# Kernel optimization log

Hardware: AMD Instinct MI355X
Metric: run time of the kernel (lower is better)

Reference implementation:

```python
import jax, jax.numpy as jnp
import numpy as np

TEMPERATURE = 8.0  # sqrt(d_k) with d_k = 64


def setup_inputs() -> dict:
    key = jax.random.key(0)
    k1, k2, k3, k4 = jax.random.split(key, 4)
    B, S, D = 16, 2048, 64  # B = batch * n_heads
    q = jax.random.normal(k1, (B, S, D), dtype=jnp.float32)
    k = jax.random.normal(k2, (B, S, D), dtype=jnp.float32)
    v = jax.random.normal(k3, (B, S, D), dtype=jnp.float32)
    # boolean mask: True = masked out. Low prob so no row is fully masked.
    mask = jax.random.uniform(k4, (B, S, S)) < 0.1
    return {"q": q, "k": k, "v": v, "mask": mask}


def reference(q, k, v, mask):
    # attn = (q @ k^T) / temperature, masked_fill(mask, -inf), softmax over last dim
    attn = jnp.einsum("bqd,bkd->bqk", q, k) / TEMPERATURE
    attn = jnp.where(mask, -jnp.inf, attn)
    attn = jax.nn.softmax(attn, axis=2)
    output = jnp.einsum("bqk,bkd->bqd", attn, v)
    return output, attn
```

## Files before the change

### kernel.cpp

```cpp
#include <hip/hip_runtime.h>

typedef _Float16 half8 __attribute__((ext_vector_type(8)));
typedef _Float16 half4 __attribute__((ext_vector_type(4)));
typedef float    floatx4 __attribute__((ext_vector_type(4)));

#define NB  16
#define SEQ 2048
#define DIM 64

#define MFMA(a,b,c) __builtin_amdgcn_mfma_f32_16x16x32_f16((a),(b),(c),0,0,0)

__global__ __launch_bounds__(256) void cvt_qk_kernel(const float* __restrict__ q,
                                                     const float* __restrict__ k,
                                                     _Float16* __restrict__ qh,
                                                     _Float16* __restrict__ kh) {
    size_t i = ((size_t)blockIdx.x * 256 + threadIdx.x) * 4;
    float4 a = *(const float4*)(q + i);
    float4 b = *(const float4*)(k + i);
    half4 ha = { (_Float16)a.x, (_Float16)a.y, (_Float16)a.z, (_Float16)a.w };
    half4 hb = { (_Float16)b.x, (_Float16)b.y, (_Float16)b.z, (_Float16)b.w };
    *(half4*)(qh + i) = ha;
    *(half4*)(kh + i) = hb;
}

__global__ __launch_bounds__(256) void cvt_vt_kernel(const float* __restrict__ v,
                                                     _Float16* __restrict__ vt) {
    __shared__ float tile[64][65];
    const int b  = blockIdx.x >> 5;
    const int s0 = (blockIdx.x & 31) << 6;
    const int t  = threadIdx.x;
    {
        const int row = t >> 2;
        const int c0  = (t & 3) << 4;
        const float* src = v + ((size_t)(b * SEQ + s0 + row)) * DIM + c0;
        #pragma unroll
        for (int i = 0; i < 4; ++i) {
            float4 x = *(const float4*)(src + i * 4);
            tile[row][c0 + i*4 + 0] = x.x;
            tile[row][c0 + i*4 + 1] = x.y;
            tile[row][c0 + i*4 + 2] = x.z;
            tile[row][c0 + i*4 + 3] = x.w;
        }
    }
    __syncthreads();
    {
        const int d  = t >> 2;
        const int sb = (t & 3) << 4;
        _Float16* dst = vt + ((size_t)(b * DIM + d)) * SEQ + s0 + sb;
        #pragma unroll
        for (int i = 0; i < 4; ++i) {
            half4 h = { (_Float16)tile[sb + i*4 + 0][d],
                        (_Float16)tile[sb + i*4 + 1][d],
                        (_Float16)tile[sb + i*4 + 2][d],
                        (_Float16)tile[sb + i*4 + 3][d] };
            *(half4*)(dst + i*4) = h;
        }
    }
}

__global__ __launch_bounds__(256) void mask_bits_kernel(const int* __restrict__ mask,
                                                        unsigned int* __restrict__ bits) {
    const int wave = threadIdx.x >> 6;
    const int lane = threadIdx.x & 63;
    const size_t row = (size_t)blockIdx.x * 4 + wave;
    const int* mp = mask + row * SEQ + lane;
    unsigned int keep = 0;
    #pragma unroll
    for (int it = 0; it < 32; ++it) {
        int m = __builtin_nontemporal_load(mp + it * 64);
        unsigned long long bal = __ballot(m != 0);
        unsigned int half = (lane & 1) ? (unsigned int)(bal >> 32) : (unsigned int)bal;
        if ((lane >> 1) == it) keep = half;
    }
    bits[row * 64 + lane] = keep;
}

__global__ __launch_bounds__(256, 8) void attn_kernel(
    const _Float16* __restrict__ qh, const _Float16* __restrict__ kh,
    const _Float16* __restrict__ vt, const unsigned int* __restrict__ bits,
    float* __restrict__ out, float* __restrict__ attn)
{
    __shared__ float wsum[4][16];
    __shared__ __align__(16) unsigned char lds_u[4 * 16 * 68 * 4];
    _Float16* tsc    = (_Float16*)lds_u;
    float*    outred = (float*)lds_u;

    const int b    = blockIdx.x >> 7;
    const int r0   = (blockIdx.x & 127) << 4;
    const int lane = threadIdx.x & 63;
    const int wave = threadIdx.x >> 6;
    const int rl   = lane & 15;
    const int g    = lane >> 4;

    const size_t qoff = ((size_t)(b * SEQ + r0 + rl)) * DIM + g * 8;
    const half8 qa0 = *(const half8*)(qh + qoff);
    const half8 qa1 = *(const half8*)(qh + qoff + 32);

    const _Float16* kbase = kh + (size_t)b * SEQ * DIM + (size_t)rl * DIM + g * 8;
    const unsigned int* bbase = bits + ((size_t)(b * SEQ + r0 + rl)) * 64 + wave;

    float rs = 0.f;
    unsigned int pb = bbase[0];

    for (int cc = 0; cc < 16; ++cc) {
        const int jj = (cc * 4 + wave) * 32;
        const unsigned int bm = pb;
        if (cc < 15) pb = bbase[(cc + 1) * 4];
        const _Float16* kp = kbase + (size_t)jj * DIM;
        half8 ka0 = *(const half8*)(kp);
        half8 ka1 = *(const half8*)(kp + 32);
        half8 kb0 = *(const half8*)(kp + 16 * DIM);
        half8 kb1 = *(const half8*)(kp + 16 * DIM + 32);
        floatx4 c0 = {0.f,0.f,0.f,0.f}, c1 = {0.f,0.f,0.f,0.f};
        c0 = MFMA(ka0, qa0, c0);
        c0 = MFMA(ka1, qa1, c0);
        c1 = MFMA(kb0, qa0, c1);
        c1 = MFMA(kb1, qa1, c1);
        const unsigned int blo = bm >> (g * 4);
        const unsigned int bhi = bm >> (g * 4 + 16);
        float e0 = (blo & 1u) ? 0.f : __expf(c0[0] * 0.125f);
        float e1 = (blo & 2u) ? 0.f : __expf(c0[1] * 0.125f);
        float e2 = (blo & 4u) ? 0.f : __expf(c0[2] * 0.125f);
        float e3 = (blo & 8u) ? 0.f : __expf(c0[3] * 0.125f);
        float e4 = (bhi & 1u) ? 0.f : __expf(c1[0] * 0.125f);
        float e5 = (bhi & 2u) ? 0.f : __expf(c1[1] * 0.125f);
        float e6 = (bhi & 4u) ? 0.f : __expf(c1[2] * 0.125f);
        float e7 = (bhi & 8u) ? 0.f : __expf(c1[3] * 0.125f);
        rs += (e0 + e1) + (e2 + e3) + (e4 + e5) + (e6 + e7);
    }

    rs += __shfl_xor(rs, 16);
    rs += __shfl_xor(rs, 32);
    if (g == 0) wsum[wave][rl] = rs;
    __syncthreads();
    const float inv = 1.0f / (wsum[0][rl] + wsum[1][rl] + wsum[2][rl] + wsum[3][rl]);

    floatx4 o0 = {0.f,0.f,0.f,0.f}, o1 = {0.f,0.f,0.f,0.f};
    floatx4 o2 = {0.f,0.f,0.f,0.f}, o3 = {0.f,0.f,0.f,0.f};
    const _Float16* vbase = vt + ((size_t)b * DIM + rl) * SEQ + g * 8;
    float* abase = attn + ((size_t)(b * SEQ + r0 + rl)) * SEQ + g * 4;
    _Float16* trow = tsc + (wave * 16 + rl) * 40;

    for (int cc = 0; cc < 16; ++cc) {
        const int jj = (cc * 4 + wave) * 32;
        const unsigned int bm = bbase[cc * 4];
        const _Float16* kp = kbase + (size_t)jj * DIM;
        half8 ka0 = *(const half8*)(kp);
        half8 ka1 = *(const half8*)(kp + 32);
        half8 kb0 = *(const half8*)(kp + 16 * DIM);
        half8 kb1 = *(const half8*)(kp + 16 * DIM + 32);
        floatx4 c0 = {0.f,0.f,0.f,0.f}, c1 = {0.f,0.f,0.f,0.f};
        c0 = MFMA(ka0, qa0, c0);
        c0 = MFMA(ka1, qa1, c0);
        c1 = MFMA(kb0, qa0, c1);
        c1 = MFMA(kb1, qa1, c1);

        const unsigned int blo = bm >> (g * 4);
        const unsigned int bhi = bm >> (g * 4 + 16);
        float e0 = (blo & 1u) ? 0.f : __expf(c0[0] * 0.125f);
        float e1 = (blo & 2u) ? 0.f : __expf(c0[1] * 0.125f);
        float e2 = (blo & 4u) ? 0.f : __expf(c0[2] * 0.125f);
        float e3 = (blo & 8u) ? 0.f : __expf(c0[3] * 0.125f);
        float e4 = (bhi & 1u) ? 0.f : __expf(c1[0] * 0.125f);
        float e5 = (bhi & 2u) ? 0.f : __expf(c1[1] * 0.125f);
        float e6 = (bhi & 4u) ? 0.f : __expf(c1[2] * 0.125f);
        float e7 = (bhi & 8u) ? 0.f : __expf(c1[3] * 0.125f);

        floatx4 a0 = { e0 * inv, e1 * inv, e2 * inv, e3 * inv };
        floatx4 a1 = { e4 * inv, e5 * inv, e6 * inv, e7 * inv };
        *(floatx4*)(abase + jj)      = a0;
        *(floatx4*)(abase + jj + 16) = a1;

        half4 h0 = { (_Float16)e0, (_Float16)e1, (_Float16)e2, (_Float16)e3 };
        half4 h1 = { (_Float16)e4, (_Float16)e5, (_Float16)e6, (_Float16)e7 };
        *(half4*)(trow + g * 4)      = h0;
        *(half4*)(trow + 16 + g * 4) = h1;
        half8 eb = *(const half8*)(trow + g * 8);

        const _Float16* vp = vbase + jj;
        half8 v0 = *(const half8*)(vp);
        half8 v1 = *(const half8*)(vp + 16 * SEQ);
        half8 v2 = *(const half8*)(vp + 32 * SEQ);
        half8 v3 = *(const half8*)(vp + 48 * SEQ);
        o0 = MFMA(v0, eb, o0);
        o1 = MFMA(v1, eb, o1);
        o2 = MFMA(v2, eb, o2);
        o3 = MFMA(v3, eb, o3);
    }

    __syncthreads();
    {
        float* orow = outred + (wave * 16 + rl) * 68 + g * 4;
        *(floatx4*)(orow +  0) = o0;
        *(floatx4*)(orow + 16) = o1;
        *(floatx4*)(orow + 32) = o2;
        *(floatx4*)(orow + 48) = o3;
    }
    __syncthreads();
    {
        const int r  = threadIdx.x >> 4;
        const int c4 = (threadIdx.x & 15) << 2;
        floatx4 s0 = *(const floatx4*)(outred + ( 0 + r) * 68 + c4);
        floatx4 s1 = *(const floatx4*)(outred + (16 + r) * 68 + c4);
        floatx4 s2 = *(const floatx4*)(outred + (32 + r) * 68 + c4);
        floatx4 s3 = *(const floatx4*)(outred + (48 + r) * 68 + c4);
        floatx4 s = (s0 + s1) + (s2 + s3);
        const float inv2 = 1.0f / (wsum[0][r] + wsum[1][r] + wsum[2][r] + wsum[3][r]);
        floatx4 ov = { s[0] * inv2, s[1] * inv2, s[2] * inv2, s[3] * inv2 };
        *(floatx4*)(out + ((size_t)(b * SEQ + r0 + r)) * DIM + c4) = ov;
    }
}

extern "C" void kernel_launch(void* const* d_in, const int* in_sizes, int n_in,
                              void* d_out, int out_size, void* d_ws, size_t ws_size,
                              hipStream_t stream) {
    const float* q = (const float*)d_in[0];
    const float* k = (const float*)d_in[1];
    const float* v = (const float*)d_in[2];
    const int* mask = (const int*)d_in[3];

    float* out  = (float*)d_out;
    float* attn = out + (size_t)NB * SEQ * DIM;

    _Float16* qh = (_Float16*)d_ws;
    _Float16* kh = qh + (size_t)NB * SEQ * DIM;
    _Float16* vt = kh + (size_t)NB * SEQ * DIM;
    unsigned int* bits = (unsigned int*)(vt + (size_t)NB * SEQ * DIM);

    cvt_qk_kernel<<<(NB * SEQ * DIM) / 1024, 256, 0, stream>>>(q, k, qh, kh);
    cvt_vt_kernel<<<NB * (SEQ / 64), 256, 0, stream>>>(v, vt);
    mask_bits_kernel<<<(NB * SEQ) / 4, 256, 0, stream>>>(mask, bits);
    attn_kernel<<<NB * (SEQ / 16), 256, 0, stream>>>(qh, kh, vt, bits, out, attn);
}
```

Baseline: 623.8 us.

## Move PV accumulation into first pass using 16x16x16 MFMA, drop LDS transpose

The P·V product is now accumulated in the first (row-sum) pass, with unnormalized fp16 exponentials fed directly from the QK accumulator layout into 16x16x16 MFMAs. This removes the per-iteration LDS round-trip that shuffled scores into operand layout, and leaves the second pass only writing normalized attention probabilities. It also remaps block indices so neighbouring blocks take different batches, and lowers the occupancy hint from 8 to 6. In exchange it uses more registers and twice as many smaller MFMA instructions, and the first pass now also loads V.

```diff
diff --git a/kernel.cpp b/kernel.cpp
--- a/kernel.cpp
+++ b/kernel.cpp
@@ -8,7 +8,8 @@
 #define SEQ 2048
 #define DIM 64
 
-#define MFMA(a,b,c) __builtin_amdgcn_mfma_f32_16x16x32_f16((a),(b),(c),0,0,0)
+#define MFMA32(a,b,c) __builtin_amdgcn_mfma_f32_16x16x32_f16((a),(b),(c),0,0,0)
+#define MFMA16(a,b,c) __builtin_amdgcn_mfma_f32_16x16x16f16((a),(b),(c),0,0,0)
 
 __global__ __launch_bounds__(256) void cvt_qk_kernel(const float* __restrict__ q,
                                                      const float* __restrict__ k,
@@ -75,18 +76,17 @@
     bits[row * 64 + lane] = keep;
 }
 
-__global__ __launch_bounds__(256, 8) void attn_kernel(
+__global__ __launch_bounds__(256, 6) void attn_kernel(
     const _Float16* __restrict__ qh, const _Float16* __restrict__ kh,
     const _Float16* __restrict__ vt, const unsigned int* __restrict__ bits,
     float* __restrict__ out, float* __restrict__ attn)
 {
     __shared__ float wsum[4][16];
-    __shared__ __align__(16) unsigned char lds_u[4 * 16 * 68 * 4];
-    _Float16* tsc    = (_Float16*)lds_u;
-    float*    outred = (float*)lds_u;
-
-    const int b    = blockIdx.x >> 7;
-    const int r0   = (blockIdx.x & 127) << 4;
+    __shared__ __align__(16) float outred[4][16][68];
+
+    const int blk  = ((blockIdx.x & 7) << 8) + (blockIdx.x >> 3);
+    const int b    = blk >> 7;
+    const int r0   = (blk & 127) << 4;
     const int lane = threadIdx.x & 63;
     const int wave = threadIdx.x >> 6;
     const int rl   = lane & 15;
@@ -97,9 +97,12 @@
     const half8 qa1 = *(const half8*)(qh + qoff + 32);
 
     const _Float16* kbase = kh + (size_t)b * SEQ * DIM + (size_t)rl * DIM + g * 8;
+    const _Float16* vbase = vt + ((size_t)b * DIM + rl) * SEQ + g * 4;
     const unsigned int* bbase = bits + ((size_t)(b * SEQ + r0 + rl)) * 64 + wave;
 
     float rs = 0.f;
+    floatx4 o0 = {0.f,0.f,0.f,0.f}, o1 = {0.f,0.f,0.f,0.f};
+    floatx4 o2 = {0.f,0.f,0.f,0.f}, o3 = {0.f,0.f,0.f,0.f};
     unsigned int pb = bbase[0];
 
     for (int cc = 0; cc < 16; ++cc) {
@@ -112,10 +115,10 @@
         half8 kb0 = *(const half8*)(kp + 16 * DIM);
         half8 kb1 = *(const half8*)(kp + 16 * DIM + 32);
         floatx4 c0 = {0.f,0.f,0.f,0.f}, c1 = {0.f,0.f,0.f,0.f};
-        c0 = MFMA(ka0, qa0, c0);
-        c0 = MFMA(ka1, qa1, c0);
-        c1 = MFMA(kb0, qa0, c1);
-        c1 = MFMA(kb1, qa1, c1);
+        c0 = MFMA32(ka0, qa0, c0);
+        c0 = MFMA32(ka1, qa1, c0);
+        c1 = MFMA32(kb0, qa0, c1);
+        c1 = MFMA32(kb1, qa1, c1);
         const unsigned int blo = bm >> (g * 4);
         const unsigned int bhi = bm >> (g * 4 + 16);
         float e0 = (blo & 1u) ? 0.f : __expf(c0[0] * 0.125f);
@@ -127,6 +130,27 @@
         float e6 = (bhi & 4u) ? 0.f : __expf(c1[2] * 0.125f);
         float e7 = (bhi & 8u) ? 0.f : __expf(c1[3] * 0.125f);
         rs += (e0 + e1) + (e2 + e3) + (e4 + e5) + (e6 + e7);
+
+        half4 h0 = { (_Float16)e0, (_Float16)e1, (_Float16)e2, (_Float16)e3 };
+        half4 h1 = { (_Float16)e4, (_Float16)e5, (_Float16)e6, (_Float16)e7 };
+
+        const _Float16* vp = vbase + jj;
+        half4 va00 = *(const half4*)(vp);
+        half4 va01 = *(const half4*)(vp + 16);
+        half4 va10 = *(const half4*)(vp + 16 * SEQ);
+        half4 va11 = *(const half4*)(vp + 16 * SEQ + 16);
+        half4 va20 = *(const half4*)(vp + 32 * SEQ);
+        half4 va21 = *(const half4*)(vp + 32 * SEQ + 16);
+        half4 va30 = *(const half4*)(vp + 48 * SEQ);
+        half4 va31 = *(const half4*)(vp + 48 * SEQ + 16);
+        o0 = MFMA16(va00, h0, o0);
+        o0 = MFMA16(va01, h1, o0);
+        o1 = MFMA16(va10, h0, o1);
+        o1 = MFMA16(va11, h1, o1);
+        o2 = MFMA16(va20, h0, o2);
+        o2 = MFMA16(va21, h1, o2);
+        o3 = MFMA16(va30, h0, o3);
+        o3 = MFMA16(va31, h1, o3);
     }
 
     rs += __shfl_xor(rs, 16);
@@ -135,11 +159,7 @@
     __syncthreads();
     const float inv = 1.0f / (wsum[0][rl] + wsum[1][rl] + wsum[2][rl] + wsum[3][rl]);
 
-    floatx4 o0 = {0.f,0.f,0.f,0.f}, o1 = {0.f,0.f,0.f,0.f};
-    floatx4 o2 = {0.f,0.f,0.f,0.f}, o3 = {0.f,0.f,0.f,0.f};
-    const _Float16* vbase = vt + ((size_t)b * DIM + rl) * SEQ + g * 8;
     float* abase = attn + ((size_t)(b * SEQ + r0 + rl)) * SEQ + g * 4;
-    _Float16* trow = tsc + (wave * 16 + rl) * 40;
 
     for (int cc = 0; cc < 16; ++cc) {
         const int jj = (cc * 4 + wave) * 32;
@@ -150,10 +170,10 @@
         half8 kb0 = *(const half8*)(kp + 16 * DIM);
         half8 kb1 = *(const half8*)(kp + 16 * DIM + 32);
         floatx4 c0 = {0.f,0.f,0.f,0.f}, c1 = {0.f,0.f,0.f,0.f};
-        c0 = MFMA(ka0, qa0, c0);
-        c0 = MFMA(ka1, qa1, c0);
-        c1 = MFMA(kb0, qa0, c1);
-        c1 = MFMA(kb1, qa1, c1);
+        c0 = MFMA32(ka0, qa0, c0);
+        c0 = MFMA32(ka1, qa1, c0);
+        c1 = MFMA32(kb0, qa0, c1);
+        c1 = MFMA32(kb1, qa1, c1);
 
         const unsigned int blo = bm >> (g * 4);
         const unsigned int bhi = bm >> (g * 4 + 16);
@@ -170,27 +190,10 @@
         floatx4 a1 = { e4 * inv, e5 * inv, e6 * inv, e7 * inv };
         *(floatx4*)(abase + jj)      = a0;
         *(floatx4*)(abase + jj + 16) = a1;
-
-        half4 h0 = { (_Float16)e0, (_Float16)e1, (_Float16)e2, (_Float16)e3 };
-        half4 h1 = { (_Float16)e4, (_Float16)e5, (_Float16)e6, (_Float16)e7 };
-        *(half4*)(trow + g * 4)      = h0;
-        *(half4*)(trow + 16 + g * 4) = h1;
-        half8 eb = *(const half8*)(trow + g * 8);
-
-        const _Float16* vp = vbase + jj;
-        half8 v0 = *(const half8*)(vp);
-        half8 v1 = *(const half8*)(vp + 16 * SEQ);
-        half8 v2 = *(const half8*)(vp + 32 * SEQ);
-        half8 v3 = *(const half8*)(vp + 48 * SEQ);
-        o0 = MFMA(v0, eb, o0);
-        o1 = MFMA(v1, eb, o1);
-        o2 = MFMA(v2, eb, o2);
-        o3 = MFMA(v3, eb, o3);
-    }
-
-    __syncthreads();
-    {
-        float* orow = outred + (wave * 16 + rl) * 68 + g * 4;
+    }
+
+    {
+        float* orow = &outred[wave][rl][g * 4];
         *(floatx4*)(orow +  0) = o0;
         *(floatx4*)(orow + 16) = o1;
         *(floatx4*)(orow + 32) = o2;
@@ -200,10 +203,10 @@
     {
         const int r  = threadIdx.x >> 4;
         const int c4 = (threadIdx.x & 15) << 2;
-        floatx4 s0 = *(const floatx4*)(outred + ( 0 + r) * 68 + c4);
-        floatx4 s1 = *(const floatx4*)(outred + (16 + r) * 68 + c4);
-        floatx4 s2 = *(const floatx4*)(outred + (32 + r) * 68 + c4);
-        floatx4 s3 = *(const floatx4*)(outred + (48 + r) * 68 + c4);
+        floatx4 s0 = *(const floatx4*)(&outred[0][r][c4]);
+        floatx4 s1 = *(const floatx4*)(&outred[1][r][c4]);
+        floatx4 s2 = *(const floatx4*)(&outred[2][r][c4]);
+        floatx4 s3 = *(const floatx4*)(&outred[3][r][c4]);
         floatx4 s = (s0 + s1) + (s2 + s3);
         const float inv2 = 1.0f / (wsum[0][r] + wsum[1][r] + wsum[2][r] + wsum[3][r]);
         floatx4 ov = { s[0] * inv2, s[1] * inv2, s[2] * inv2, s[3] * inv2 };
```

Result: slower. 667.1 us (+6.9%).
